# Optimization experiments

Hardware: AMD Instinct MI355X
Metric: run time of the kernel (lower is better)

## Reference

```python
import jax, jax.numpy as jnp
import numpy as np

NBIT = 8


def _qmm(x, W, key):
    """Bit-serial quantized matmul with per-bit noisy weights (faithful to torch quantization()).
    x: (..., in), W: (out, in). Returns z (..., out), min, max, last noisy weight."""
    nsplit = 2 ** NBIT - 1
    mn = jnp.min(x)
    mx = jnp.max(x)
    q = ((x - mn) / (mx - mn) * nsplit).astype(jnp.uint8)  # trunc cast like torch .type(uint8)
    z = jnp.zeros(x.shape[:-1] + (W.shape[0],), x.dtype)
    Wn = W
    for i in range(NBIT):  # fixed 8-bit loop
        noise = jax.random.normal(jax.random.fold_in(key, i), W.shape, W.dtype) * jnp.abs(W) * 0.1
        Wn = W + noise
        bit = ((q >> i) & 1).astype(x.dtype) * float(2 ** i)
        z = z + jnp.matmul(bit, Wn.T)
    return z, mn, mx, Wn  # Wn = weight left in fc after loop (last bit's noisy weight)


def _requant(z, mn, mx, W_last):
    nsplit = 2 ** NBIT - 1
    bias = jnp.sum(mn * W_last, axis=1)  # (out,)
    return z / nsplit * (mx - mn) + bias


def _bn(x2d, gamma, beta, eps=1e-5):
    m = x2d.mean(axis=0)
    v = x2d.var(axis=0)  # biased, like torch BN training normalization
    return (x2d - m) / jnp.sqrt(v + eps) * gamma + beta


def _forward(node_embedding, edge_embedding, nbr_mask, c_two, c_two2, c_three, c_three2,
             bn2_g, bn2_b, bn3_g, bn3_b, nbr_idx):
    B, At, Nbr, Fe = edge_embedding.shape
    Fn = node_embedding.shape[-1]
    gather = jax.vmap(lambda x, i: x[i])  # batched fancy gather along atom axis
    key = jax.random.key(42)

    # two-body
    node_i = jnp.broadcast_to(node_embedding[:, :, None, :], (B, At, Nbr, Fn))
    node_j = gather(node_embedding, nbr_idx) * nbr_mask[..., None]  # (B,At,Nbr,Fn)
    c2 = jnp.concatenate([node_i, node_j], axis=3)  # (B,At,Nbr,2Fn)
    z, mn, mx, Wl = _qmm(c2, c_two, jax.random.fold_in(key, 0))
    c2 = jax.nn.relu(_requant(z, mn, mx, Wl))
    z, mn, mx, Wl = _qmm(c2, c_two2, jax.random.fold_in(key, 1))
    c2 = _requant(z, mn, mx, Wl)
    g2, e2 = jnp.split(c2, 2, axis=3)
    two = jax.nn.sigmoid(g2) * jnp.tanh(e2)
    two = _bn(two.reshape(-1, Fe), bn2_g, bn2_b).reshape(B, At, Nbr, Fe)

    # three-body
    nbr_jk = gather(nbr_idx, nbr_idx)                 # (B,At,Nbr,Nbr) neighbors-of-neighbors
    node_k = gather(node_embedding, nbr_jk)           # (B,At,Nbr,Nbr,Fn)
    edge_jk = gather(edge_embedding, nbr_idx)         # (B,At,Nbr,Nbr,Fe)
    edge_ij = jnp.broadcast_to(edge_embedding[:, :, :, None, :], (B, At, Nbr, Nbr, Fe))
    c3 = jnp.concatenate([
        jnp.broadcast_to(node_i[:, :, :, None, :], (B, At, Nbr, Nbr, Fn)),
        jnp.broadcast_to(node_j[:, :, :, None, :], (B, At, Nbr, Nbr, Fn)),
        node_k, edge_ij, edge_jk], axis=4)            # (B,At,Nbr,Nbr,3Fn+2Fe)
    z, mn, mx, Wl = _qmm(c3, c_three, jax.random.fold_in(key, 2))
    c3 = jax.nn.relu(_requant(z, mn, mx, Wl))
    z, mn, mx, Wl = _qmm(c3, c_three2, jax.random.fold_in(key, 3))
    c3 = _requant(z, mn, mx, Wl)
    g3, e3 = jnp.split(c3, 2, axis=4)
    three = jax.nn.sigmoid(g3) * jnp.tanh(e3)
    mask_jk = gather(nbr_mask, nbr_idx)               # (B,At,Nbr,Nbr) = nbr_mask[b, nbr_idx[b,i,j], k]
    three = (three * mask_jk[..., None]).sum(axis=3)  # (B,At,Nbr,Fe)
    three = _bn(three.reshape(-1, Fe), bn3_g, bn3_b).reshape(B, At, Nbr, Fe)

    return jax.nn.relu(edge_embedding + two + three)


def setup_inputs() -> dict:
    key = jax.random.key(0)
    ks = jax.random.split(key, 8)
    B, At, Nbr, Fn, Fe = 4, 48, 20, 64, 64
    return {
        "node_embedding": jax.random.normal(ks[0], (B, At, Fn), jnp.float32),
        "edge_embedding": jax.random.normal(ks[1], (B, At, Nbr, Fe), jnp.float32),
        "nbr_mask": jnp.ones((B, At, Nbr), jnp.float32),
        "c_two": jax.random.normal(ks[2], (8 * Fn, 2 * Fn), jnp.float32) * 0.05,
        "c_two2": jax.random.normal(ks[3], (2 * Fe, 8 * Fn), jnp.float32) * 0.05,
        "c_three": jax.random.normal(ks[4], (6 * Fn + 4 * Fe, 3 * Fn + 2 * Fe), jnp.float32) * 0.05,
        "c_three2": jax.random.normal(ks[5], (2 * Fe, 6 * Fn + 4 * Fe), jnp.float32) * 0.05,
        "bn2_g": jnp.ones((Fe,), jnp.float32),
        "bn2_b": jnp.zeros((Fe,), jnp.float32),
        "bn3_g": jnp.ones((Fe,), jnp.float32),
        "bn3_b": jnp.zeros((Fe,), jnp.float32),
        "nbr_idx": jax.random.randint(ks[6], (B, At, Nbr), 0, At, jnp.int32),
    }


def reference(node_embedding, edge_embedding, nbr_mask, c_two, c_two2, c_three, c_three2,
              bn2_g, bn2_b, bn3_g, bn3_b, nbr_idx):
    return _forward(node_embedding, edge_embedding, nbr_mask, c_two, c_two2, c_three, c_three2,
                    bn2_g, bn2_b, bn3_g, bn3_b, nbr_idx)
```

## Files before the change

kernel.cpp:

```cpp
#include <hip/hip_runtime.h>
#include <cstdint>
#include <cstddef>

#define DEVI __device__ __forceinline__

typedef __attribute__((ext_vector_type(8))) short s8v;
typedef __attribute__((ext_vector_type(4))) float f4v;

static constexpr int B_ = 4, AT = 48, NBRS = 20;
static constexpr int R2 = B_ * AT * NBRS;
static constexpr int M4 = R2 * NBRS;

static constexpr size_t OFF_B2A  = 0;
static constexpr size_t OFF_B2B  = OFF_B2A + 524288;
static constexpr size_t OFF_B3A  = OFF_B2B + 524288;
static constexpr size_t OFF_BW3B = OFF_B3A + 1638400;
static constexpr size_t OFF_BN3B = OFF_BW3B + 81920;
static constexpr size_t OFF_W72A = OFF_BN3B + 327680;
static constexpr size_t OFF_W72B = OFF_W72A + 65536;
static constexpr size_t OFF_W73A = OFF_W72B + 65536;
static constexpr size_t OFF_W73B = OFF_W73A + 204800;
static constexpr size_t OFF_RS   = OFF_W73B + 81920;
static constexpr size_t OFF_SLOT = OFF_RS + 1408;
static constexpr size_t OFF_BN   = OFF_SLOT + 16;
static constexpr size_t OFF_C2IN = OFF_BN + 256;
static constexpr size_t OFF_Z1   = OFF_C2IN + (size_t)R2 * 128;
static constexpr size_t OFF_C2B  = OFF_Z1 + (size_t)R2 * 512;
static constexpr size_t OFF_Z2   = OFF_C2B + (size_t)R2 * 512;
static constexpr size_t OFF_TWO  = OFF_Z2 + (size_t)R2 * 128;
static constexpr size_t OFF_NK   = OFF_TWO + (size_t)R2 * 64;
static constexpr size_t OFF_P2   = OFF_NK + (size_t)R2 * 64;
static constexpr size_t OFF_P3   = OFF_P2 + (size_t)R2 * 640;
static constexpr size_t OFF_TSUM = OFF_P3 + (size_t)R2 * 640;
static constexpr size_t OFF_Q2A  = OFF_TSUM + (size_t)R2 * 64;
static constexpr size_t OFF_Q2B  = OFF_Q2A + 122880;
static constexpr size_t OFF_QP2  = OFF_Q2B + 491520;
static constexpr size_t OFF_QP3  = OFF_QP2 + 184320;

DEVI void tf2x32(unsigned k0, unsigned k1, unsigned x0, unsigned x1,
                 unsigned& o0, unsigned& o1) {
  unsigned ks0 = k0, ks1 = k1, ks2 = k0 ^ k1 ^ 0x1BD11BDAu;
  x0 += ks0; x1 += ks1;
  const unsigned rotA[4] = {13u, 15u, 26u, 6u};
  const unsigned rotB[4] = {17u, 29u, 16u, 24u};
  unsigned ks[3] = {ks0, ks1, ks2};
  #pragma unroll
  for (int i = 0; i < 5; ++i) {
    const unsigned* rot = (i & 1) ? rotB : rotA;
    #pragma unroll
    for (int r = 0; r < 4; ++r) {
      x0 += x1;
      x1 = (x1 << rot[r]) | (x1 >> (32u - rot[r]));
      x1 ^= x0;
    }
    x0 += ks[(i + 1) % 3];
    x1 += ks[(i + 2) % 3] + (unsigned)(i + 1);
  }
  o0 = x0; o1 = x1;
}

DEVI float erfinv_xla(float x) {
  float w = -log1pf(-x * x);
  float p;
  if (w < 5.f) {
    w -= 2.5f;
    p = 2.81022636e-08f;
    p = fmaf(p, w, 3.43273939e-07f);
    p = fmaf(p, w, -3.5233877e-06f);
    p = fmaf(p, w, -4.39150654e-06f);
    p = fmaf(p, w, 0.00021858087f);
    p = fmaf(p, w, -0.00125372503f);
    p = fmaf(p, w, -0.00417768164f);
    p = fmaf(p, w, 0.246640727f);
    p = fmaf(p, w, 1.50140941f);
  } else {
    w = sqrtf(w) - 3.f;
    p = -0.000200214257f;
    p = fmaf(p, w, 0.000100950558f);
    p = fmaf(p, w, 0.00134934322f);
    p = fmaf(p, w, -0.00367342844f);
    p = fmaf(p, w, 0.00573950773f);
    p = fmaf(p, w, -0.0076224613f);
    p = fmaf(p, w, 0.00943887047f);
    p = fmaf(p, w, 1.00167406f);
    p = fmaf(p, w, 2.83297682f);
  }
  return p * x;
}

DEVI float normal_from_bits(unsigned bits) {
  unsigned fb = (bits >> 9) | 0x3F800000u;
  float f = __uint_as_float(fb) - 1.0f;
  const float lo = -0.99999994f;
  float u = f * (1.0f - lo) + lo;
  u = fmaxf(lo, u);
  return 1.41421356237f * erfinv_xla(u);
}

DEVI unsigned f2o(float f) { unsigned u = __float_as_uint(f); return (u & 0x80000000u) ? ~u : (u | 0x80000000u); }
DEVI float o2f(unsigned u) { return (u & 0x80000000u) ? __uint_as_float(u & 0x7FFFFFFFu) : __uint_as_float(~u); }

DEVI unsigned short f2bf(float x) {
  unsigned u = __float_as_uint(x);
  return (unsigned short)((u + 0x7FFFu + ((u >> 16) & 1u)) >> 16);
}
DEVI float bf2f(unsigned short h) { return __uint_as_float((unsigned)h << 16); }

DEVI void blockMinMax(float lmn, float lmx, float* smem, unsigned* slot) {
  float* smn = smem; float* smx = smem + 256;
  int t = threadIdx.x;
  smn[t] = lmn; smx[t] = lmx;
  __syncthreads();
  for (int s = 128; s > 0; s >>= 1) {
    if (t < s) { smn[t] = fminf(smn[t], smn[t + s]); smx[t] = fmaxf(smx[t], smx[t + s]); }
    __syncthreads();
  }
  if (t == 0) { atomicMin(slot + 0, f2o(smn[0])); atomicMax(slot + 1, f2o(smx[0])); }
}

DEVI s8v expand_mul(unsigned b) {
  unsigned sl = (b & 15u) * 0x00204081u;
  unsigned sh = ((b >> 4) & 15u) * 0x00204081u;
  union { unsigned u[4]; s8v s; } r;
  r.u[0] = (sl & 0x00010001u) * 0x3F80u;
  r.u[1] = ((sl >> 8) & 0x00010001u) * 0x3F80u;
  r.u[2] = (sh & 0x00010001u) * 0x3F80u;
  r.u[3] = ((sh >> 8) & 0x00010001u) * 0x3F80u;
  return r.s;
}
DEVI constexpr int bperm(int bit) { return bit ^ ((((bit) ^ (bit >> 1)) & 1) * 3); }

DEVI s8v bytes_to_bf16(unsigned a, unsigned b) {
  union { unsigned u[4]; s8v s; } r;
  float f0 = (float)(a & 255u), f1 = (float)((a >> 8) & 255u);
  float f2 = (float)((a >> 16) & 255u), f3 = (float)(a >> 24);
  r.u[0] = (__float_as_uint(f0) >> 16) | (__float_as_uint(f1) & 0xFFFF0000u);
  r.u[1] = (__float_as_uint(f2) >> 16) | (__float_as_uint(f3) & 0xFFFF0000u);
  f0 = (float)(b & 255u); f1 = (float)((b >> 8) & 255u);
  f2 = (float)((b >> 16) & 255u); f3 = (float)(b >> 24);
  r.u[2] = (__float_as_uint(f0) >> 16) | (__float_as_uint(f1) & 0xFFFF0000u);
  r.u[3] = (__float_as_uint(f2) >> 16) | (__float_as_uint(f3) & 0xFFFF0000u);
  return r.s;
}

__global__ __launch_bounds__(256) void k_prep(
    const float* __restrict__ W2A, const float* __restrict__ W2B,
    const float* __restrict__ W3A, const float* __restrict__ W3B,
    short* __restrict__ B2A, short* __restrict__ B2B, short* __restrict__ B3A,
    short* __restrict__ BW3B, short* __restrict__ BN3B,
    float* __restrict__ W72A, float* __restrict__ W72B,
    float* __restrict__ W73A, float* __restrict__ W73B,
    float* __restrict__ z1, float* __restrict__ z2, float* __restrict__ tsum,
    unsigned* __restrict__ slots) {
  int t = blockIdx.x * 256 + threadIdx.x;
  if (t < R2 * 512) z1[t] = 0.f;
  if (t < R2 * 128) z2[t] = 0.f;
  if (t < R2 * 64) tsum[t] = 0.f;
  if (t < 4) { slots[2 * t] = f2o(3.402823466e38f); slots[2 * t + 1] = f2o(-3.402823466e38f); }
  int lt = t;
  const float* W; float* W7; int N, K; unsigned layer; int which;
  if (lt < 65536) { W = W2A; W7 = W72A; N = 512; K = 128; layer = 0u; which = 0; }
  else if ((lt -= 65536) < 65536) { W = W2B; W7 = W72B; N = 128; K = 512; layer = 1u; which = 1; }
  else if ((lt -= 65536) < 204800) { W = W3A; W7 = W73A; N = 640; K = 320; layer = 2u; which = 2; }
  else if ((lt -= 204800) < 81920) { W = W3B; W7 = W73B; N = 128; K = 640; layer = 3u; which = 3; }
  else return;
  int e = lt;
  int n = e / K, k = e - n * K;
  float w = W[e];
  float aw = fabsf(w) * 0.1f;
  unsigned kl0, kl1;
  tf2x32(0u, 42u, 0u, layer, kl0, kl1);
  union { short s[8]; s8v v; } hv, lv, bnv;
  #pragma unroll
  for (int bit = 0; bit < 8; ++bit) {
    unsigned kb0, kb1, r0, r1;
    tf2x32(kl0, kl1, 0u, (unsigned)bit, kb0, kb1);
    tf2x32(kb0, kb1, 0u, (unsigned)e, r0, r1);
    float nz = normal_from_bits(r0 ^ r1) * aw;
    float wn = w + nz;
    if (bit == 7) W7[e] = wn;
    if (which == 3) {
      bnv.s[bperm(bit)] = (short)f2bf(ldexpf(nz, bit));
    } else {
      float sv = ldexpf(wn, bit);
      unsigned short hi = f2bf(sv);
      unsigned short lo = f2bf(sv - bf2f(hi));
      hv.s[bperm(bit)] = (short)hi;
      lv.s[bperm(bit)] = (short)lo;
    }
  }
  if (which == 3) {
    *(s8v*)(BN3B + ((size_t)(n >> 4) * 160 + (size_t)(k >> 2)) * 512
                 + (size_t)((k & 3) * 16 + (n & 15)) * 8) = bnv.v;
    unsigned short hi = f2bf(w);
    unsigned short lo = f2bf(w - bf2f(hi));
    size_t o2 = (((size_t)(n >> 4) * 20 + (size_t)(k >> 5)) * 2) * 512
              + (size_t)(((k >> 3) & 3) * 16 + (n & 15)) * 8 + (k & 7);
    BW3B[o2] = (short)hi; BW3B[o2 + 512] = (short)lo;
  } else {
    int pk = k;
    if (which == 2) {
      if (k >= 128 && k < 192) pk = k + 64;
      else if (k >= 192 && k < 256) pk = k - 64;
    }
    short* Bf = (which == 0) ? B2A : (which == 1 ? B2B : B3A);
    int KG = K >> 2;
    size_t off = (((size_t)(n >> 4) * KG + (size_t)(pk >> 2)) * 2) * 512
               + (size_t)((pk & 3) * 16 + (n & 15)) * 8;
    *(s8v*)(Bf + off) = hv.v;
    *(s8v*)(Bf + off + 512) = lv.v;
  }
}

__global__ __launch_bounds__(256) void k_build2(
    const float* __restrict__ node, const float* __restrict__ mask,
    const int* __restrict__ nidx, float* __restrict__ c2in, float* __restrict__ NK,
    const float* __restrict__ W72A, const float* __restrict__ W72B,
    const float* __restrict__ W73A, const float* __restrict__ W73B,
    float* __restrict__ rs, unsigned* __restrict__ slot) {
  __shared__ float sred[512];
  int idx = blockIdx.x * 256 + threadIdx.x;
  float lmn = 3.4e38f, lmx = -3.4e38f;
  if (idx < R2 * 128) {
    int row = idx >> 7, c = idx & 127;
    float v;
    if (c < 64) v = node[(size_t)(row / 20) * 64 + c];
    else {
      int b = row / 960;
      v = node[(size_t)(b * 48 + nidx[row]) * 64 + (c - 64)] * mask[row];
    }
    c2in[idx] = v; lmn = v; lmx = v;
  } else if (idx < R2 * 192) {
    int i2 = idx - R2 * 128;
    int row = i2 >> 6, c = i2 & 63;
    int b = row / 960;
    NK[i2] = node[(size_t)(b * 48 + nidx[row]) * 64 + c];
  } else if (idx < R2 * 192 + 1408) {
    int o = idx - R2 * 192;
    const float* p; int cols; int dsto;
    if (o < 512) { p = W72A; cols = 128; dsto = o; }
    else if (o < 640) { p = W72B; cols = 512; dsto = o; o -= 512; }
    else if (o < 1280) { p = W73A; cols = 320; dsto = o; o -= 640; }
    else { p = W73B; cols = 640; dsto = o; o -= 1280; }
    const float* rowp = p + (size_t)o * cols;
    float s = 0.f;
    for (int j = 0; j < cols; ++j) s += rowp[j];
    rs[dsto] = s;
  }
  blockMinMax(lmn, lmx, sred, slot);
}

__global__ __launch_bounds__(256) void k_qm4(
    const float* __restrict__ node, const float* __restrict__ edge,
    const float* __restrict__ c2in, const float* __restrict__ NK,
    const int* __restrict__ nidx, const unsigned* __restrict__ slot0,
    unsigned char* __restrict__ Q2A, unsigned* __restrict__ slot4) {
  __shared__ float sred[512];
  int idx0 = blockIdx.x * 256 + threadIdx.x;
  if (idx0 < R2 * 128) {
    const float mn = o2f(slot0[0]), mx = o2f(slot0[1]);
    float invd = 255.f / (mx - mn);
    Q2A[idx0] = (unsigned char)((c2in[idx0] - mn) * invd);
  }
  const int n0 = 12288, n1 = n0 + 245760, n2 = n1 + 245760, total = n2 + 4915200;
  float lmn = 3.4e38f, lmx = -3.4e38f;
  for (int idx = idx0; idx < total; idx += gridDim.x * 256) {
    float v, v2;
    if (idx < n0) { v = node[idx]; v2 = v; }
    else if (idx < n1) { v = edge[idx - n0]; v2 = v; }
    else if (idx < n2) {
      int j = idx - n1; int r = j >> 6, c = j & 63;
      v = c2in[(size_t)r * 128 + 64 + c]; v2 = v;
    } else {
      int j = idx - n2; int bij = j / 1280, t = j - bij * 1280;
      int b = bij / 960;
      size_t base = (size_t)((b * 48 + nidx[bij]) * 20) * 64 + t;
      v = NK[base]; v2 = edge[base];
    }
    lmn = fminf(lmn, fminf(v, v2)); lmx = fmaxf(lmx, fmaxf(v, v2));
  }
  blockMinMax(lmn, lmx, sred, slot4);
}

__global__ __launch_bounds__(256) void k_mfma_gemm(
    const unsigned char* __restrict__ Q, int ldq,
    const short* __restrict__ B, int KGfull, int kg0,
    int M, int Nfull, int KB, float* __restrict__ Z, int accflag) {
  const int tid = threadIdx.x;
  const int lane = tid & 63, w = tid >> 6;
  const int l15 = lane & 15, l4 = lane >> 4;
  const int mbase = blockIdx.y * 64;
  const int nbase = blockIdx.x * 128;
  const int kq0 = blockIdx.z * KB;
  f4v acc[4][2];
  #pragma unroll
  for (int a = 0; a < 4; ++a)
    #pragma unroll
    for (int b = 0; b < 2; ++b) acc[a][b] = f4v{0.f, 0.f, 0.f, 0.f};
  for (int ks16 = 0; ks16 < KB; ks16 += 16) {
    uint4 qv[4];
    #pragma unroll
    for (int mf = 0; mf < 4; ++mf)
      qv[mf] = *(const uint4*)(Q + (size_t)(mbase + mf * 16 + l15) * ldq + kq0 + ks16);
    #pragma unroll
    for (int sub = 0; sub < 4; ++sub) {
      int kg = kg0 + ((kq0 + ks16) >> 2) + sub;
      s8v af[4];
      #pragma unroll
      for (int mf = 0; mf < 4; ++mf) {
        unsigned wv = (sub == 0) ? qv[mf].x : (sub == 1) ? qv[mf].y : (sub == 2) ? qv[mf].z : qv[mf].w;
        af[mf] = expand_mul((wv >> (l4 * 8)) & 255u);
      }
      #pragma unroll
      for (int j = 0; j < 2; ++j) {
        size_t o = (((size_t)(nbase / 16 + w * 2 + j) * KGfull + kg) * 2) * 512 + (size_t)lane * 8;
        s8v bh = *(const s8v*)(B + o);
        s8v bl = *(const s8v*)(B + o + 512);
        #pragma unroll
        for (int mf = 0; mf < 4; ++mf) {
          acc[mf][j] = __builtin_amdgcn_mfma_f32_16x16x32_bf16(af[mf], bh, acc[mf][j], 0, 0, 0);
          acc[mf][j] = __builtin_amdgcn_mfma_f32_16x16x32_bf16(af[mf], bl, acc[mf][j], 0, 0, 0);
        }
      }
    }
  }
  #pragma unroll
  for (int mf = 0; mf < 4; ++mf) {
    #pragma unroll
    for (int r = 0; r < 4; ++r) {
      int m = mbase + mf * 16 + l4 * 4 + r;
      float* zp = Z + (size_t)m * Nfull + nbase;
      #pragma unroll
      for (int j = 0; j < 2; ++j) {
        int n = (w * 2 + j) * 16 + l15;
        if (accflag == 0) zp[n] = acc[mf][j][r];
        else atomicAdd(zp + n, acc[mf][j][r]);
      }
    }
  }
}

__global__ __launch_bounds__(256) void k_act1(const float* __restrict__ z1, const float* __restrict__ rs,
                                              const unsigned* __restrict__ slot0,
                                              unsigned* __restrict__ slot1) {
  __shared__ float sred[512];
  const float mn = o2f(slot0[0]), mx = o2f(slot0[1]);
  int idx = blockIdx.x * 256 + threadIdx.x;
  float lmn = 3.4e38f, lmx = -3.4e38f;
  if (idx < R2 * 512) {
    int o = idx & 511;
    float v = fmaxf(0.f, z1[idx] * (1.f / 255.f) * (mx - mn) + mn * rs[o]);
    lmn = v; lmx = v;
  }
  blockMinMax(lmn, lmx, sred, slot1);
}

__global__ __launch_bounds__(256) void k_qq(
    const float* __restrict__ z1, const float* __restrict__ rs,
    const float* __restrict__ node, const float* __restrict__ edge,
    const float* __restrict__ c2in, const float* __restrict__ NK,
    const int* __restrict__ nidx, const unsigned* __restrict__ slot0,
    const unsigned* __restrict__ slot2, const unsigned* __restrict__ slot4,
    unsigned char* __restrict__ Q2B, unsigned char* __restrict__ QP2, unsigned char* __restrict__ QP3) {
  int idx = blockIdx.x * 256 + threadIdx.x;
  if (idx < R2 * 512) {
    const float mn0 = o2f(slot0[0]), mx0 = o2f(slot0[1]);
    const float mn = o2f(slot2[0]), mx = o2f(slot2[1]);
    int o = idx & 511;
    float v = fmaxf(0.f, z1[idx] * (1.f / 255.f) * (mx0 - mn0) + mn0 * rs[o]);
    Q2B[idx] = (unsigned char)((v - mn) * (255.f / (mx - mn)));
    return;
  }
  int j = idx - R2 * 512;
  const int seg = 245760;
  if (j >= 5 * seg) return;
  const float mn = o2f(slot4[0]), mx = o2f(slot4[1]);
  const float invd = 255.f / (mx - mn);
  int s = j / seg; int jj = j - s * seg;
  int r = jj >> 6, c = jj & 63;
  float v; unsigned char* dst;
  if (s == 0)      { v = node[(size_t)(r / 20) * 64 + c];  dst = QP2 + (size_t)r * 192 + c; }
  else if (s == 1) { v = c2in[(size_t)r * 128 + 64 + c];   dst = QP2 + (size_t)r * 192 + 64 + c; }
  else if (s == 2) { v = edge[(size_t)r * 64 + c];         dst = QP2 + (size_t)r * 192 + 128 + c; }
  else if (s == 3) { v = NK[(size_t)r * 64 + c];           dst = QP3 + (size_t)r * 128 + c; }
  else             { v = edge[(size_t)r * 64 + c];         dst = QP3 + (size_t)r * 128 + 64 + c; }
  *dst = (unsigned char)((v - mn) * invd);
}

__global__ __launch_bounds__(256) void k_mfma_p23(
    const unsigned char* __restrict__ Q2, const unsigned char* __restrict__ Q3,
    const short* __restrict__ B, float* __restrict__ P2, float* __restrict__ P3) {
  const int half = blockIdx.y >= 60;
  const int by = blockIdx.y - half * 60;
  const unsigned char* Q = half ? Q3 : Q2;
  float* Z = half ? P3 : P2;
  const int kg0 = half ? 48 : 0;
  const int KB = half ? 128 : 192;
  const int ldq = half ? 128 : 192;
  const int tid = threadIdx.x;
  const int lane = tid & 63, w = tid >> 6;
  const int l15 = lane & 15, l4 = lane >> 4;
  const int mbase = by * 64;
  const int nbase = blockIdx.x * 128;
  f4v acc[4][2];
  #pragma unroll
  for (int a = 0; a < 4; ++a)
    #pragma unroll
    for (int b = 0; b < 2; ++b) acc[a][b] = f4v{0.f, 0.f, 0.f, 0.f};
  for (int ks16 = 0; ks16 < KB; ks16 += 16) {
    uint4 qv[4];
    #pragma unroll
    for (int mf = 0; mf < 4; ++mf)
      qv[mf] = *(const uint4*)(Q + (size_t)(mbase + mf * 16 + l15) * ldq + ks16);
    #pragma unroll
    for (int sub = 0; sub < 4; ++sub) {
      int kg = kg0 + (ks16 >> 2) + sub;
      s8v af[4];
      #pragma unroll
      for (int mf = 0; mf < 4; ++mf) {
        unsigned wv = (sub == 0) ? qv[mf].x : (sub == 1) ? qv[mf].y : (sub == 2) ? qv[mf].z : qv[mf].w;
        af[mf] = expand_mul((wv >> (l4 * 8)) & 255u);
      }
      #pragma unroll
      for (int j = 0; j < 2; ++j) {
        size_t o = (((size_t)(nbase / 16 + w * 2 + j) * 80 + kg) * 2) * 512 + (size_t)lane * 8;
        s8v bh = *(const s8v*)(B + o);
        s8v bl = *(const s8v*)(B + o + 512);
        #pragma unroll
        for (int mf = 0; mf < 4; ++mf) {
          acc[mf][j] = __builtin_amdgcn_mfma_f32_16x16x32_bf16(af[mf], bh, acc[mf][j], 0, 0, 0);
          acc[mf][j] = __builtin_amdgcn_mfma_f32_16x16x32_bf16(af[mf], bl, acc[mf][j], 0, 0, 0);
        }
      }
    }
  }
  #pragma unroll
  for (int mf = 0; mf < 4; ++mf) {
    #pragma unroll
    for (int r = 0; r < 4; ++r) {
      int m = mbase + mf * 16 + l4 * 4 + r;
      float* zp = Z + (size_t)m * 640 + nbase;
      #pragma unroll
      for (int j = 0; j < 2; ++j)
        zp[(w * 2 + j) * 16 + l15] = acc[mf][j][r];
    }
  }
}

__global__ __launch_bounds__(256) void k_act2mm3(
    const float* __restrict__ z2, const float* __restrict__ rs2b,
    const unsigned* __restrict__ slot2, float* __restrict__ two,
    const float* __restrict__ P12, const float* __restrict__ P3,
    const float* __restrict__ rs3a, const int* __restrict__ nidx,
    const unsigned* __restrict__ slot4, unsigned* __restrict__ slot6) {
  __shared__ float p12s[640];
  __shared__ float bias[640];
  __shared__ float sred[512];
  int gid = blockIdx.x * 256 + threadIdx.x;
  if (gid < R2 * 64) {
    const float mn = o2f(slot2[0]), mx = o2f(slot2[1]);
    int row = gid >> 6, c = gid & 63;
    float d = (mx - mn) * (1.f / 255.f);
    float g = z2[(size_t)row * 128 + c] * d + mn * rs2b[c];
    float e = z2[(size_t)row * 128 + 64 + c] * d + mn * rs2b[64 + c];
    two[gid] = (1.f / (1.f + expf(-g))) * tanhf(e);
  }
  const int bij = blockIdx.x;
  const int b = bij / 960;
  const int jp = nidx[bij];
  const size_t p3b = (size_t)((b * 48 + jp) * 20) * 640;
  const float mn2 = o2f(slot4[0]), mx2 = o2f(slot4[1]);
  const float sc2 = (mx2 - mn2) * (1.f / 255.f);
  for (int k = threadIdx.x; k < 640; k += 256) {
    p12s[k] = P12[(size_t)bij * 640 + k];
    bias[k] = mn2 * rs3a[k];
  }
  __syncthreads();
  float lmn = 3.4e38f, lmx = -3.4e38f;
  for (int t = threadIdx.x; t < 20 * 640; t += 256) {
    int knb = t / 640, k = t - knb * 640;
    float v = fmaxf(0.f, (p12s[k] + P3[p3b + t]) * sc2 + bias[k]);
    lmn = fminf(lmn, v); lmx = fmaxf(lmx, v);
  }
  blockMinMax(lmn, lmx, sred, slot6);
}

__global__ __launch_bounds__(256) void k_mfma_l3b(
    const float* __restrict__ P12, const float* __restrict__ P3,
    const float* __restrict__ rs3a, const float* __restrict__ rs3b,
    const short* __restrict__ BW, const short* __restrict__ BN,
    const int* __restrict__ nidx, const float* __restrict__ mask,
    const unsigned* __restrict__ slotA, const unsigned* __restrict__ slotB,
    float* __restrict__ tsum) {
  __shared__ unsigned char qt[64 * 648];
  const int tid = threadIdx.x;
  const int s0 = blockIdx.x * 64;
  const float mn2 = o2f(slotA[0]), mx2 = o2f(slotA[1]);
  const float mn3 = o2f(slotB[0]), mx3 = o2f(slotB[1]);
  const float sc2 = (mx2 - mn2) * (1.f / 255.f);
  const float invd3 = 255.f / (mx3 - mn3);
  {
    int r = tid >> 2, kq = (tid & 3) * 160;
    int s = s0 + r;
    int bij = s / 20, knb = s - bij * 20, b = bij / 960;
    int p3row = (b * 48 + nidx[bij]) * 20 + knb;
    const float* pa = P12 + (size_t)bij * 640;
    const float* pb = P3 + (size_t)p3row * 640;
    for (int k = kq; k < kq + 160; k += 4) {
      float4 va = *(const float4*)(pa + k);
      float4 vb = *(const float4*)(pb + k);
      float4 rv = *(const float4*)(rs3a + k);
      float v0 = fmaxf(0.f, (va.x + vb.x) * sc2 + mn2 * rv.x);
      float v1 = fmaxf(0.f, (va.y + vb.y) * sc2 + mn2 * rv.y);
      float v2 = fmaxf(0.f, (va.z + vb.z) * sc2 + mn2 * rv.z);
      float v3 = fmaxf(0.f, (va.w + vb.w) * sc2 + mn2 * rv.w);
      unsigned pk = (unsigned)((v0 - mn3) * invd3) | ((unsigned)((v1 - mn3) * invd3) << 8)
                  | ((unsigned)((v2 - mn3) * invd3) << 16) | ((unsigned)((v3 - mn3) * invd3) << 24);
      *(unsigned*)(&qt[(size_t)r * 648 + k]) = pk;
    }
  }
  __syncthreads();
  const int lane = tid & 63, wave = tid >> 6;
  const int wm = wave >> 1, wn = wave & 1;
  const int l15 = lane & 15, l4 = lane >> 4;
  const int nfl[4] = {2 * wn, 2 * wn + 1, 2 * wn + 4, 2 * wn + 5};
  size_t bb[4];
  #pragma unroll
  for (int j = 0; j < 4; ++j) bb[j] = ((size_t)nfl[j] * 160) * 512 + (size_t)lane * 8;
  f4v acc[2][4];
  #pragma unroll
  for (int a = 0; a < 2; ++a)
    #pragma unroll
    for (int b = 0; b < 4; ++b) acc[a][b] = f4v{0.f, 0.f, 0.f, 0.f};
  s8v c0[4], c1[4];
  #pragma unroll
  for (int j = 0; j < 4; ++j) {
    c0[j] = *(const s8v*)(BN + bb[j]);
    c1[j] = *(const s8v*)(BN + bb[j] + 512);
  }
  const unsigned char* qrow0 = &qt[(size_t)(wm * 32 + l15) * 648];
  const unsigned char* qrow1 = qrow0 + 16 * 648;
  for (int c = 0; c < 20; ++c) {
    s8v bwh[4];
    #pragma unroll
    for (int j = 0; j < 4; ++j)
      bwh[j] = *(const s8v*)(BW + (((size_t)nfl[j] * 20 + c) * 2) * 512 + (size_t)lane * 8);
    #pragma unroll
    for (int s = 0; s < 8; ++s) {
      const int kg = c * 8 + s;
      unsigned w0 = *(const unsigned*)(qrow0 + kg * 4);
      unsigned w1 = *(const unsigned*)(qrow1 + kg * 4);
      s8v af0 = expand_mul((w0 >> (l4 * 8)) & 255u);
      s8v af1 = expand_mul((w1 >> (l4 * 8)) & 255u);
      s8v nx[4];
      #pragma unroll
      for (int j = 0; j < 4; ++j)
        nx[j] = *(const s8v*)(BN + bb[j] + (size_t)(kg + 2) * 512);
      __builtin_amdgcn_s_setprio(1);
      #pragma unroll
      for (int j = 0; j < 4; ++j) {
        acc[0][j] = __builtin_amdgcn_mfma_f32_16x16x32_bf16(af0, c0[j], acc[0][j], 0, 0, 0);
        acc[1][j] = __builtin_amdgcn_mfma_f32_16x16x32_bf16(af1, c0[j], acc[1][j], 0, 0, 0);
      }
      __builtin_amdgcn_s_setprio(0);
      #pragma unroll
      for (int j = 0; j < 4; ++j) { c0[j] = c1[j]; c1[j] = nx[j]; }
    }
    {
      const int x = c * 32 + l4 * 8;
      unsigned a0 = *(const unsigned*)(qrow0 + x);
      unsigned a1 = *(const unsigned*)(qrow0 + x + 4);
      s8v aq0 = bytes_to_bf16(a0, a1);
      a0 = *(const unsigned*)(qrow1 + x);
      a1 = *(const unsigned*)(qrow1 + x + 4);
      s8v aq1 = bytes_to_bf16(a0, a1);
      __builtin_amdgcn_s_setprio(1);
      #pragma unroll
      for (int j = 0; j < 4; ++j) {
        acc[0][j] = __builtin_amdgcn_mfma_f32_16x16x32_bf16(aq0, bwh[j], acc[0][j], 0, 0, 0);
        acc[1][j] = __builtin_amdgcn_mfma_f32_16x16x32_bf16(aq1, bwh[j], acc[1][j], 0, 0, 0);
        s8v bwl = *(const s8v*)(BW + ((((size_t)nfl[j] * 20 + c) * 2) + 1) * 512 + (size_t)lane * 8);
        acc[0][j] = __builtin_amdgcn_mfma_f32_16x16x32_bf16(aq0, bwl, acc[0][j], 0, 0, 0);
        acc[1][j] = __builtin_amdgcn_mfma_f32_16x16x32_bf16(aq1, bwl, acc[1][j], 0, 0, 0);
      }
      __builtin_amdgcn_s_setprio(0);
    }
  }
  const float d3 = (mx3 - mn3) * (1.f / 255.f);
  float rg[2], re[2];
  #pragma unroll
  for (int j = 0; j < 2; ++j) {
    int gcol = (2 * wn + j) * 16 + l15;
    rg[j] = mn3 * rs3b[gcol];
    re[j] = mn3 * rs3b[64 + gcol];
  }
  #pragma unroll
  for (int mf = 0; mf < 2; ++mf) {
    #pragma unroll
    for (int r = 0; r < 4; ++r) {
      int s = s0 + wm * 32 + mf * 16 + l4 * 4 + r;
      int bij = s / 20, knb = s - bij * 20, b = bij / 960;
      int p3row = (b * 48 + nidx[bij]) * 20 + knb;
      float mk = mask[p3row];
      #pragma unroll
      for (int j = 0; j < 2; ++j) {
        float g = acc[mf][j][r] * d3 + rg[j];
        float e = acc[mf][j + 2][r] * d3 + re[j];
        float val = (1.f / (1.f + expf(-g))) * tanhf(e) * mk;
        atomicAdd(&tsum[(size_t)bij * 64 + (2 * wn + j) * 16 + l15], val);
      }
    }
  }
}

__global__ __launch_bounds__(256) void k_bnstats2(const float* __restrict__ two, const float* __restrict__ tsum,
                                                  float* __restrict__ bn) {
  __shared__ float ss[512];
  const float* x = blockIdx.y ? tsum : two;
  float* mout = bn + (blockIdx.y ? 128 : 0);
  float* vout = mout + 64;
  int c = blockIdx.x, t = threadIdx.x;
  float s = 0.f, q = 0.f;
  for (int r = t; r < R2; r += 256) { float v = x[(size_t)r * 64 + c]; s += v; q += v * v; }
  ss[t] = s; ss[256 + t] = q;
  __syncthreads();
  for (int st = 128; st > 0; st >>= 1) {
    if (t < st) { ss[t] += ss[t + st]; ss[256 + t] += ss[256 + t + st]; }
    __syncthreads();
  }
  if (t == 0) { float m = ss[0] / (float)R2; mout[c] = m; vout[c] = ss[256] / (float)R2 - m * m; }
}

__global__ __launch_bounds__(256) void k_final(const float* __restrict__ edge, const float* __restrict__ two,
                                               const float* __restrict__ tsum, const float* __restrict__ bn,
                                               const float* __restrict__ g2, const float* __restrict__ b2,
                                               const float* __restrict__ g3, const float* __restrict__ b3,
                                               float* __restrict__ out) {
  int idx = blockIdx.x * 256 + threadIdx.x;
  if (idx >= R2 * 64) return;
  int c = idx & 63;
  float t2 = (two[idx] - bn[c]) / sqrtf(bn[64 + c] + 1e-5f) * g2[c] + b2[c];
  float t3 = (tsum[idx] - bn[128 + c]) / sqrtf(bn[192 + c] + 1e-5f) * g3[c] + b3[c];
  out[idx] = fmaxf(0.f, edge[idx] + t2 + t3);
}

extern "C" void kernel_launch(void* const* d_in, const int* in_sizes, int n_in,
                              void* d_out, int out_size, void* d_ws, size_t ws_size,
                              hipStream_t stream) {
  (void)in_sizes; (void)n_in; (void)out_size; (void)ws_size;
  const float* node   = (const float*)d_in[0];
  const float* edge   = (const float*)d_in[1];
  const float* mask   = (const float*)d_in[2];
  const float* c_two  = (const float*)d_in[3];
  const float* c_two2 = (const float*)d_in[4];
  const float* c_three  = (const float*)d_in[5];
  const float* c_three2 = (const float*)d_in[6];
  const float* bn2g = (const float*)d_in[7];
  const float* bn2b = (const float*)d_in[8];
  const float* bn3g = (const float*)d_in[9];
  const float* bn3b = (const float*)d_in[10];
  const int*   nidx = (const int*)d_in[11];
  float* ws = (float*)d_ws;
  unsigned* slots = (unsigned*)(ws + OFF_SLOT);
  float* out = (float*)d_out;
  short* B2A  = (short*)(ws + OFF_B2A);
  short* B2B  = (short*)(ws + OFF_B2B);
  short* B3A  = (short*)(ws + OFF_B3A);
  short* BW3B = (short*)(ws + OFF_BW3B);
  short* BN3B = (short*)(ws + OFF_BN3B);
  unsigned char* Q2A = (unsigned char*)(ws + OFF_Q2A);
  unsigned char* Q2B = (unsigned char*)(ws + OFF_Q2B);
  unsigned char* QP2 = (unsigned char*)(ws + OFF_QP2);
  unsigned char* QP3 = (unsigned char*)(ws + OFF_QP3);
  float* RS = ws + OFF_RS;

  k_prep<<<7680, 256, 0, stream>>>(c_two, c_two2, c_three, c_three2,
                                   B2A, B2B, B3A, BW3B, BN3B,
                                   ws + OFF_W72A, ws + OFF_W72B, ws + OFF_W73A, ws + OFF_W73B,
                                   ws + OFF_Z1, ws + OFF_Z2, ws + OFF_TSUM, slots);
  k_build2<<<2886, 256, 0, stream>>>(node, mask, nidx, ws + OFF_C2IN, ws + OFF_NK,
                                     ws + OFF_W72A, ws + OFF_W72B, ws + OFF_W73A, ws + OFF_W73B,
                                     RS, slots + 0);
  k_qm4<<<2048, 256, 0, stream>>>(node, edge, ws + OFF_C2IN, ws + OFF_NK, nidx, slots + 0,
                                  Q2A, slots + 4);
  k_mfma_gemm<<<dim3(4, 60, 2), 256, 0, stream>>>(Q2A, 128, B2A, 32, 0, 3840, 512, 64, ws + OFF_Z1, 3);
  k_act1<<<7680, 256, 0, stream>>>(ws + OFF_Z1, RS, slots + 0, slots + 2);
  k_qq<<<12480, 256, 0, stream>>>(ws + OFF_Z1, RS, node, edge, ws + OFF_C2IN, ws + OFF_NK,
                                  nidx, slots + 0, slots + 2, slots + 4, Q2B, QP2, QP3);
  k_mfma_gemm<<<dim3(1, 60, 4), 256, 0, stream>>>(Q2B, 512, B2B, 128, 0, 3840, 128, 128, ws + OFF_Z2, 3);
  k_mfma_p23<<<dim3(5, 120), 256, 0, stream>>>(QP2, QP3, B3A, ws + OFF_P2, ws + OFF_P3);
  k_act2mm3<<<3840, 256, 0, stream>>>(ws + OFF_Z2, RS + 512, slots + 2, ws + OFF_TWO,
                                      ws + OFF_P2, ws + OFF_P3, RS + 640, nidx, slots + 4, slots + 6);
  k_mfma_l3b<<<1200, 256, 0, stream>>>(ws + OFF_P2, ws + OFF_P3, RS + 640, RS + 1280,
                                       BW3B, BN3B, nidx, mask, slots + 4, slots + 6, ws + OFF_TSUM);
  k_bnstats2<<<dim3(64, 2), 256, 0, stream>>>(ws + OFF_TWO, ws + OFF_TSUM, ws + OFF_BN);
  k_final<<<960, 256, 0, stream>>>(edge, ws + OFF_TWO, ws + OFF_TSUM, ws + OFF_BN,
                                   bn2g, bn2b, bn3g, bn3b, out);
}
```

Before: 807.6 us.

## Split bit-serial weights into noise-only bf16 and shared hi/lo base for all GEMMs

Applies to the first three quantized matmuls the decomposition already used in layer 3b. Each per-bit noisy weight becomes a noise-only bf16 term per bit plus one shared hi/lo bf16 base weight multiplied by the full byte value. This replaces the old hi+lo MFMA pair for every bit with one MFMA per bit plus a few base MFMAs, roughly halving matrix work. It also merges the p23 kernel into two launches of a generic kernel and removes s_setprio hints in l3b. The cost is one more launch, a different precision profile (the noise term is rounded to bf16 alone), and a changed wave tiling.

```diff
diff --git a/kernel.cpp b/kernel.cpp
--- a/kernel.cpp
+++ b/kernel.cpp
@@ -11,12 +11,15 @@
 static constexpr int R2 = B_ * AT * NBRS;
 static constexpr int M4 = R2 * NBRS;
 
-static constexpr size_t OFF_B2A  = 0;
-static constexpr size_t OFF_B2B  = OFF_B2A + 524288;
-static constexpr size_t OFF_B3A  = OFF_B2B + 524288;
-static constexpr size_t OFF_BW3B = OFF_B3A + 1638400;
-static constexpr size_t OFF_BN3B = OFF_BW3B + 81920;
-static constexpr size_t OFF_W72A = OFF_BN3B + 327680;
+static constexpr size_t OFF_BN2A = 0;
+static constexpr size_t OFF_BW2A = OFF_BN2A + 262144;
+static constexpr size_t OFF_BN2B = OFF_BW2A + 65536;
+static constexpr size_t OFF_BW2B = OFF_BN2B + 262144;
+static constexpr size_t OFF_BN3A = OFF_BW2B + 65536;
+static constexpr size_t OFF_BW3A = OFF_BN3A + 819200;
+static constexpr size_t OFF_BN3B = OFF_BW3A + 204800;
+static constexpr size_t OFF_BW3B = OFF_BN3B + 327680;
+static constexpr size_t OFF_W72A = OFF_BW3B + 81920;
 static constexpr size_t OFF_W72B = OFF_W72A + 65536;
 static constexpr size_t OFF_W73A = OFF_W72B + 65536;
 static constexpr size_t OFF_W73B = OFF_W73A + 204800;
@@ -25,8 +28,7 @@
 static constexpr size_t OFF_BN   = OFF_SLOT + 16;
 static constexpr size_t OFF_C2IN = OFF_BN + 256;
 static constexpr size_t OFF_Z1   = OFF_C2IN + (size_t)R2 * 128;
-static constexpr size_t OFF_C2B  = OFF_Z1 + (size_t)R2 * 512;
-static constexpr size_t OFF_Z2   = OFF_C2B + (size_t)R2 * 512;
+static constexpr size_t OFF_Z2   = OFF_Z1 + (size_t)R2 * 512;
 static constexpr size_t OFF_TWO  = OFF_Z2 + (size_t)R2 * 128;
 static constexpr size_t OFF_NK   = OFF_TWO + (size_t)R2 * 64;
 static constexpr size_t OFF_P2   = OFF_NK + (size_t)R2 * 64;
@@ -146,8 +148,10 @@
 __global__ __launch_bounds__(256) void k_prep(
     const float* __restrict__ W2A, const float* __restrict__ W2B,
     const float* __restrict__ W3A, const float* __restrict__ W3B,
-    short* __restrict__ B2A, short* __restrict__ B2B, short* __restrict__ B3A,
-    short* __restrict__ BW3B, short* __restrict__ BN3B,
+    short* __restrict__ BN2A, short* __restrict__ BW2A,
+    short* __restrict__ BN2B, short* __restrict__ BW2B,
+    short* __restrict__ BN3A, short* __restrict__ BW3A,
+    short* __restrict__ BN3B, short* __restrict__ BW3B,
     float* __restrict__ W72A, float* __restrict__ W72B,
     float* __restrict__ W73A, float* __restrict__ W73B,
     float* __restrict__ z1, float* __restrict__ z2, float* __restrict__ tsum,
@@ -158,11 +162,11 @@
   if (t < R2 * 64) tsum[t] = 0.f;
   if (t < 4) { slots[2 * t] = f2o(3.402823466e38f); slots[2 * t + 1] = f2o(-3.402823466e38f); }
   int lt = t;
-  const float* W; float* W7; int N, K; unsigned layer; int which;
-  if (lt < 65536) { W = W2A; W7 = W72A; N = 512; K = 128; layer = 0u; which = 0; }
-  else if ((lt -= 65536) < 65536) { W = W2B; W7 = W72B; N = 128; K = 512; layer = 1u; which = 1; }
-  else if ((lt -= 65536) < 204800) { W = W3A; W7 = W73A; N = 640; K = 320; layer = 2u; which = 2; }
-  else if ((lt -= 204800) < 81920) { W = W3B; W7 = W73B; N = 128; K = 640; layer = 3u; which = 3; }
+  const float* W; float* W7; short* BNp; short* BWp; int K; unsigned layer; int which;
+  if (lt < 65536) { W = W2A; W7 = W72A; BNp = BN2A; BWp = BW2A; K = 128; layer = 0u; which = 0; }
+  else if ((lt -= 65536) < 65536) { W = W2B; W7 = W72B; BNp = BN2B; BWp = BW2B; K = 512; layer = 1u; which = 1; }
+  else if ((lt -= 65536) < 204800) { W = W3A; W7 = W73A; BNp = BN3A; BWp = BW3A; K = 320; layer = 2u; which = 2; }
+  else if ((lt -= 204800) < 81920) { W = W3B; W7 = W73B; BNp = BN3B; BWp = BW3B; K = 640; layer = 3u; which = 3; }
   else return;
   int e = lt;
   int n = e / K, k = e - n * K;
@@ -170,46 +174,28 @@
   float aw = fabsf(w) * 0.1f;
   unsigned kl0, kl1;
   tf2x32(0u, 42u, 0u, layer, kl0, kl1);
-  union { short s[8]; s8v v; } hv, lv, bnv;
+  union { short s[8]; s8v v; } bnv;
   #pragma unroll
   for (int bit = 0; bit < 8; ++bit) {
     unsigned kb0, kb1, r0, r1;
     tf2x32(kl0, kl1, 0u, (unsigned)bit, kb0, kb1);
     tf2x32(kb0, kb1, 0u, (unsigned)e, r0, r1);
     float nz = normal_from_bits(r0 ^ r1) * aw;
-    float wn = w + nz;
-    if (bit == 7) W7[e] = wn;
-    if (which == 3) {
-      bnv.s[bperm(bit)] = (short)f2bf(ldexpf(nz, bit));
-    } else {
-      float sv = ldexpf(wn, bit);
-      unsigned short hi = f2bf(sv);
-      unsigned short lo = f2bf(sv - bf2f(hi));
-      hv.s[bperm(bit)] = (short)hi;
-      lv.s[bperm(bit)] = (short)lo;
-    }
-  }
-  if (which == 3) {
-    *(s8v*)(BN3B + ((size_t)(n >> 4) * 160 + (size_t)(k >> 2)) * 512
-                 + (size_t)((k & 3) * 16 + (n & 15)) * 8) = bnv.v;
-    unsigned short hi = f2bf(w);
-    unsigned short lo = f2bf(w - bf2f(hi));
-    size_t o2 = (((size_t)(n >> 4) * 20 + (size_t)(k >> 5)) * 2) * 512
-              + (size_t)(((k >> 3) & 3) * 16 + (n & 15)) * 8 + (k & 7);
-    BW3B[o2] = (short)hi; BW3B[o2 + 512] = (short)lo;
-  } else {
-    int pk = k;
-    if (which == 2) {
-      if (k >= 128 && k < 192) pk = k + 64;
-      else if (k >= 192 && k < 256) pk = k - 64;
-    }
-    short* Bf = (which == 0) ? B2A : (which == 1 ? B2B : B3A);
-    int KG = K >> 2;
-    size_t off = (((size_t)(n >> 4) * KG + (size_t)(pk >> 2)) * 2) * 512
-               + (size_t)((pk & 3) * 16 + (n & 15)) * 8;
-    *(s8v*)(Bf + off) = hv.v;
-    *(s8v*)(Bf + off + 512) = lv.v;
-  }
+    if (bit == 7) W7[e] = w + nz;
+    bnv.s[bperm(bit)] = (short)f2bf(ldexpf(nz, bit));
+  }
+  int pk = k;
+  if (which == 2) {
+    if (k >= 128 && k < 192) pk = k + 64;
+    else if (k >= 192 && k < 256) pk = k - 64;
+  }
+  *(s8v*)(BNp + ((size_t)(n >> 4) * (K >> 2) + (size_t)(pk >> 2)) * 512
+              + (size_t)((pk & 3) * 16 + (n & 15)) * 8) = bnv.v;
+  unsigned short hi = f2bf(w);
+  unsigned short lo = f2bf(w - bf2f(hi));
+  size_t o2 = (((size_t)(n >> 4) * (K >> 5) + (size_t)(pk >> 5)) * 2) * 512
+            + (size_t)(((pk >> 3) & 3) * 16 + (n & 15)) * 8 + (pk & 7);
+  BWp[o2] = (short)hi; BWp[o2 + 512] = (short)lo;
 }
 
 __global__ __launch_bounds__(256) void k_build2(
@@ -282,57 +268,93 @@
   blockMinMax(lmn, lmx, sred, slot4);
 }
 
-__global__ __launch_bounds__(256) void k_mfma_gemm(
+__global__ __launch_bounds__(256) void k_nsgemm(
     const unsigned char* __restrict__ Q, int ldq,
-    const short* __restrict__ B, int KGfull, int kg0,
-    int M, int Nfull, int KB, float* __restrict__ Z, int accflag) {
+    const short* __restrict__ BNp, const short* __restrict__ BWp,
+    int KCfull, int c0, int Nfull, int CB,
+    float* __restrict__ Z, int accflag) {
   const int tid = threadIdx.x;
-  const int lane = tid & 63, w = tid >> 6;
+  const int lane = tid & 63, wave = tid >> 6;
+  const int wm = wave >> 1, wn = wave & 1;
   const int l15 = lane & 15, l4 = lane >> 4;
+  const int nfl[4] = {2 * wn, 2 * wn + 1, 2 * wn + 4, 2 * wn + 5};
   const int mbase = blockIdx.y * 64;
   const int nbase = blockIdx.x * 128;
-  const int kq0 = blockIdx.z * KB;
-  f4v acc[4][2];
-  #pragma unroll
-  for (int a = 0; a < 4; ++a)
-    #pragma unroll
-    for (int b = 0; b < 2; ++b) acc[a][b] = f4v{0.f, 0.f, 0.f, 0.f};
-  for (int ks16 = 0; ks16 < KB; ks16 += 16) {
-    uint4 qv[4];
-    #pragma unroll
-    for (int mf = 0; mf < 4; ++mf)
-      qv[mf] = *(const uint4*)(Q + (size_t)(mbase + mf * 16 + l15) * ldq + kq0 + ks16);
-    #pragma unroll
-    for (int sub = 0; sub < 4; ++sub) {
-      int kg = kg0 + ((kq0 + ks16) >> 2) + sub;
-      s8v af[4];
-      #pragma unroll
-      for (int mf = 0; mf < 4; ++mf) {
-        unsigned wv = (sub == 0) ? qv[mf].x : (sub == 1) ? qv[mf].y : (sub == 2) ? qv[mf].z : qv[mf].w;
-        af[mf] = expand_mul((wv >> (l4 * 8)) & 255u);
+  const int cstart = blockIdx.z * CB;
+  size_t bbn[4], bbw[4];
+  #pragma unroll
+  for (int j = 0; j < 4; ++j) {
+    size_t nf = (size_t)(nbase / 16 + nfl[j]);
+    bbn[j] = nf * ((size_t)KCfull * 8) * 512 + (size_t)lane * 8;
+    bbw[j] = nf * (size_t)KCfull * 2 * 512 + (size_t)lane * 8;
+  }
+  const unsigned char* qrow0 = Q + (size_t)(mbase + wm * 32 + l15) * ldq;
+  const unsigned char* qrow1 = qrow0 + (size_t)16 * ldq;
+  f4v acc[2][4];
+  #pragma unroll
+  for (int a = 0; a < 2; ++a)
+    #pragma unroll
+    for (int b = 0; b < 4; ++b) acc[a][b] = f4v{0.f, 0.f, 0.f, 0.f};
+  const int kgs = (cstart + c0) * 8;
+  s8v c0v[4], c1v[4];
+  #pragma unroll
+  for (int j = 0; j < 4; ++j) {
+    c0v[j] = *(const s8v*)(BNp + bbn[j] + (size_t)kgs * 512);
+    c1v[j] = *(const s8v*)(BNp + bbn[j] + (size_t)(kgs + 1) * 512);
+  }
+  for (int cl = 0; cl < CB; ++cl) {
+    const int c = cstart + cl;
+    const int cb = c + c0;
+    s8v bwh[4];
+    #pragma unroll
+    for (int j = 0; j < 4; ++j)
+      bwh[j] = *(const s8v*)(BWp + bbw[j] + (size_t)cb * 2 * 512);
+    #pragma unroll
+    for (int s = 0; s < 8; ++s) {
+      const int kg = cb * 8 + s;
+      unsigned w0 = *(const unsigned*)(qrow0 + c * 32 + s * 4);
+      unsigned w1 = *(const unsigned*)(qrow1 + c * 32 + s * 4);
+      s8v af0 = expand_mul((w0 >> (l4 * 8)) & 255u);
+      s8v af1 = expand_mul((w1 >> (l4 * 8)) & 255u);
+      s8v nx[4];
+      #pragma unroll
+      for (int j = 0; j < 4; ++j)
+        nx[j] = *(const s8v*)(BNp + bbn[j] + (size_t)(kg + 2) * 512);
+      #pragma unroll
+      for (int j = 0; j < 4; ++j) {
+        acc[0][j] = __builtin_amdgcn_mfma_f32_16x16x32_bf16(af0, c0v[j], acc[0][j], 0, 0, 0);
+        acc[1][j] = __builtin_amdgcn_mfma_f32_16x16x32_bf16(af1, c0v[j], acc[1][j], 0, 0, 0);
       }
       #pragma unroll
-      for (int j = 0; j < 2; ++j) {
-        size_t o = (((size_t)(nbase / 16 + w * 2 + j) * KGfull + kg) * 2) * 512 + (size_t)lane * 8;
-        s8v bh = *(const s8v*)(B + o);
-        s8v bl = *(const s8v*)(B + o + 512);
-        #pragma unroll
-        for (int mf = 0; mf < 4; ++mf) {
-          acc[mf][j] = __builtin_amdgcn_mfma_f32_16x16x32_bf16(af[mf], bh, acc[mf][j], 0, 0, 0);
-          acc[mf][j] = __builtin_amdgcn_mfma_f32_16x16x32_bf16(af[mf], bl, acc[mf][j], 0, 0, 0);
-        }
+      for (int j = 0; j < 4; ++j) { c0v[j] = c1v[j]; c1v[j] = nx[j]; }
+    }
+    {
+      const int x = c * 32 + l4 * 8;
+      unsigned a0 = *(const unsigned*)(qrow0 + x);
+      unsigned a1 = *(const unsigned*)(qrow0 + x + 4);
+      s8v aq0 = bytes_to_bf16(a0, a1);
+      a0 = *(const unsigned*)(qrow1 + x);
+      a1 = *(const unsigned*)(qrow1 + x + 4);
+      s8v aq1 = bytes_to_bf16(a0, a1);
+      #pragma unroll
+      for (int j = 0; j < 4; ++j) {
+        acc[0][j] = __builtin_amdgcn_mfma_f32_16x16x32_bf16(aq0, bwh[j], acc[0][j], 0, 0, 0);
+        acc[1][j] = __builtin_amdgcn_mfma_f32_16x16x32_bf16(aq1, bwh[j], acc[1][j], 0, 0, 0);
+        s8v bwl = *(const s8v*)(BWp + bbw[j] + ((size_t)cb * 2 + 1) * 512);
+        acc[0][j] = __builtin_amdgcn_mfma_f32_16x16x32_bf16(aq0, bwl, acc[0][j], 0, 0, 0);
+        acc[1][j] = __builtin_amdgcn_mfma_f32_16x16x32_bf16(aq1, bwl, acc[1][j], 0, 0, 0);
       }
     }
   }
   #pragma unroll
-  for (int mf = 0; mf < 4; ++mf) {
+  for (int mf = 0; mf < 2; ++mf) {
     #pragma unroll
     for (int r = 0; r < 4; ++r) {
-      int m = mbase + mf * 16 + l4 * 4 + r;
+      int m = mbase + wm * 32 + mf * 16 + l4 * 4 + r;
       float* zp = Z + (size_t)m * Nfull + nbase;
       #pragma unroll
-      for (int j = 0; j < 2; ++j) {
-        int n = (w * 2 + j) * 16 + l15;
+      for (int j = 0; j < 4; ++j) {
+        int n = nfl[j] * 16 + l15;
         if (accflag == 0) zp[n] = acc[mf][j][r];
         else atomicAdd(zp + n, acc[mf][j][r]);
       }
@@ -385,66 +407,6 @@
   else if (s == 3) { v = NK[(size_t)r * 64 + c];           dst = QP3 + (size_t)r * 128 + c; }
   else             { v = edge[(size_t)r * 64 + c];         dst = QP3 + (size_t)r * 128 + 64 + c; }
   *dst = (unsigned char)((v - mn) * invd);
-}
-
-__global__ __launch_bounds__(256) void k_mfma_p23(
-    const unsigned char* __restrict__ Q2, const unsigned char* __restrict__ Q3,
-    const short* __restrict__ B, float* __restrict__ P2, float* __restrict__ P3) {
-  const int half = blockIdx.y >= 60;
-  const int by = blockIdx.y - half * 60;
-  const unsigned char* Q = half ? Q3 : Q2;
-  float* Z = half ? P3 : P2;
-  const int kg0 = half ? 48 : 0;
-  const int KB = half ? 128 : 192;
-  const int ldq = half ? 128 : 192;
-  const int tid = threadIdx.x;
-  const int lane = tid & 63, w = tid >> 6;
-  const int l15 = lane & 15, l4 = lane >> 4;
-  const int mbase = by * 64;
-  const int nbase = blockIdx.x * 128;
-  f4v acc[4][2];
-  #pragma unroll
-  for (int a = 0; a < 4; ++a)
-    #pragma unroll
-    for (int b = 0; b < 2; ++b) acc[a][b] = f4v{0.f, 0.f, 0.f, 0.f};
-  for (int ks16 = 0; ks16 < KB; ks16 += 16) {
-    uint4 qv[4];
-    #pragma unroll
-    for (int mf = 0; mf < 4; ++mf)
-      qv[mf] = *(const uint4*)(Q + (size_t)(mbase + mf * 16 + l15) * ldq + ks16);
-    #pragma unroll
-    for (int sub = 0; sub < 4; ++sub) {
-      int kg = kg0 + (ks16 >> 2) + sub;
-      s8v af[4];
-      #pragma unroll
-      for (int mf = 0; mf < 4; ++mf) {
-        unsigned wv = (sub == 0) ? qv[mf].x : (sub == 1) ? qv[mf].y : (sub == 2) ? qv[mf].z : qv[mf].w;
-        af[mf] = expand_mul((wv >> (l4 * 8)) & 255u);
-      }
-      #pragma unroll
-      for (int j = 0; j < 2; ++j) {
-        size_t o = (((size_t)(nbase / 16 + w * 2 + j) * 80 + kg) * 2) * 512 + (size_t)lane * 8;
-        s8v bh = *(const s8v*)(B + o);
-        s8v bl = *(const s8v*)(B + o + 512);
-        #pragma unroll
-        for (int mf = 0; mf < 4; ++mf) {
-          acc[mf][j] = __builtin_amdgcn_mfma_f32_16x16x32_bf16(af[mf], bh, acc[mf][j], 0, 0, 0);
-          acc[mf][j] = __builtin_amdgcn_mfma_f32_16x16x32_bf16(af[mf], bl, acc[mf][j], 0, 0, 0);
-        }
-      }
-    }
-  }
-  #pragma unroll
-  for (int mf = 0; mf < 4; ++mf) {
-    #pragma unroll
-    for (int r = 0; r < 4; ++r) {
-      int m = mbase + mf * 16 + l4 * 4 + r;
-      float* zp = Z + (size_t)m * 640 + nbase;
-      #pragma unroll
-      for (int j = 0; j < 2; ++j)
-        zp[(w * 2 + j) * 16 + l15] = acc[mf][j][r];
-    }
-  }
 }
 
 __global__ __launch_bounds__(256) void k_act2mm3(
@@ -556,13 +518,11 @@
       #pragma unroll
       for (int j = 0; j < 4; ++j)
         nx[j] = *(const s8v*)(BN + bb[j] + (size_t)(kg + 2) * 512);
-      __builtin_amdgcn_s_setprio(1);
       #pragma unroll
       for (int j = 0; j < 4; ++j) {
         acc[0][j] = __builtin_amdgcn_mfma_f32_16x16x32_bf16(af0, c0[j], acc[0][j], 0, 0, 0);
         acc[1][j] = __builtin_amdgcn_mfma_f32_16x16x32_bf16(af1, c0[j], acc[1][j], 0, 0, 0);
       }
-      __builtin_amdgcn_s_setprio(0);
       #pragma unroll
       for (int j = 0; j < 4; ++j) { c0[j] = c1[j]; c1[j] = nx[j]; }
     }
@@ -574,7 +534,6 @@
       a0 = *(const unsigned*)(qrow1 + x);
       a1 = *(const unsigned*)(qrow1 + x + 4);
       s8v aq1 = bytes_to_bf16(a0, a1);
-      __builtin_amdgcn_s_setprio(1);
       #pragma unroll
       for (int j = 0; j < 4; ++j) {
         acc[0][j] = __builtin_amdgcn_mfma_f32_16x16x32_bf16(aq0, bwh[j], acc[0][j], 0, 0, 0);
@@ -583,7 +542,6 @@
         acc[0][j] = __builtin_amdgcn_mfma_f32_16x16x32_bf16(aq0, bwl, acc[0][j], 0, 0, 0);
         acc[1][j] = __builtin_amdgcn_mfma_f32_16x16x32_bf16(aq1, bwl, acc[1][j], 0, 0, 0);
       }
-      __builtin_amdgcn_s_setprio(0);
     }
   }
   const float d3 = (mx3 - mn3) * (1.f / 255.f);
@@ -663,11 +621,10 @@
   float* ws = (float*)d_ws;
   unsigned* slots = (unsigned*)(ws + OFF_SLOT);
   float* out = (float*)d_out;
-  short* B2A  = (short*)(ws + OFF_B2A);
-  short* B2B  = (short*)(ws + OFF_B2B);
-  short* B3A  = (short*)(ws + OFF_B3A);
-  short* BW3B = (short*)(ws + OFF_BW3B);
-  short* BN3B = (short*)(ws + OFF_BN3B);
+  short* BN2A = (short*)(ws + OFF_BN2A); short* BW2A = (short*)(ws + OFF_BW2A);
+  short* BN2B = (short*)(ws + OFF_BN2B); short* BW2B = (short*)(ws + OFF_BW2B);
+  short* BN3A = (short*)(ws + OFF_BN3A); short* BW3A = (short*)(ws + OFF_BW3A);
+  short* BN3B = (short*)(ws + OFF_BN3B); short* BW3B = (short*)(ws + OFF_BW3B);
   unsigned char* Q2A = (unsigned char*)(ws + OFF_Q2A);
   unsigned char* Q2B = (unsigned char*)(ws + OFF_Q2B);
   unsigned char* QP2 = (unsigned char*)(ws + OFF_QP2);
@@ -675,7 +632,7 @@
   float* RS = ws + OFF_RS;
 
   k_prep<<<7680, 256, 0, stream>>>(c_two, c_two2, c_three, c_three2,
-                                   B2A, B2B, B3A, BW3B, BN3B,
+                                   BN2A, BW2A, BN2B, BW2B, BN3A, BW3A, BN3B, BW3B,
                                    ws + OFF_W72A, ws + OFF_W72B, ws + OFF_W73A, ws + OFF_W73B,
                                    ws + OFF_Z1, ws + OFF_Z2, ws + OFF_TSUM, slots);
   k_build2<<<2886, 256, 0, stream>>>(node, mask, nidx, ws + OFF_C2IN, ws + OFF_NK,
@@ -683,12 +640,13 @@
                                      RS, slots + 0);
   k_qm4<<<2048, 256, 0, stream>>>(node, edge, ws + OFF_C2IN, ws + OFF_NK, nidx, slots + 0,
                                   Q2A, slots + 4);
-  k_mfma_gemm<<<dim3(4, 60, 2), 256, 0, stream>>>(Q2A, 128, B2A, 32, 0, 3840, 512, 64, ws + OFF_Z1, 3);
+  k_nsgemm<<<dim3(4, 60, 2), 256, 0, stream>>>(Q2A, 128, BN2A, BW2A, 4, 0, 512, 2, ws + OFF_Z1, 3);
   k_act1<<<7680, 256, 0, stream>>>(ws + OFF_Z1, RS, slots + 0, slots + 2);
   k_qq<<<12480, 256, 0, stream>>>(ws + OFF_Z1, RS, node, edge, ws + OFF_C2IN, ws + OFF_NK,
                                   nidx, slots + 0, slots + 2, slots + 4, Q2B, QP2, QP3);
-  k_mfma_gemm<<<dim3(1, 60, 4), 256, 0, stream>>>(Q2B, 512, B2B, 128, 0, 3840, 128, 128, ws + OFF_Z2, 3);
-  k_mfma_p23<<<dim3(5, 120), 256, 0, stream>>>(QP2, QP3, B3A, ws + OFF_P2, ws + OFF_P3);
+  k_nsgemm<<<dim3(1, 60, 4), 256, 0, stream>>>(Q2B, 512, BN2B, BW2B, 16, 0, 128, 4, ws + OFF_Z2, 3);
+  k_nsgemm<<<dim3(5, 60, 1), 256, 0, stream>>>(QP2, 192, BN3A, BW3A, 10, 0, 640, 6, ws + OFF_P2, 0);
+  k_nsgemm<<<dim3(5, 60, 1), 256, 0, stream>>>(QP3, 128, BN3A, BW3A, 10, 6, 640, 4, ws + OFF_P3, 0);
   k_act2mm3<<<3840, 256, 0, stream>>>(ws + OFF_Z2, RS + 512, slots + 2, ws + OFF_TWO,
                                       ws + OFF_P2, ws + OFF_P3, RS + 640, nidx, slots + 4, slots + 6);
   k_mfma_l3b<<<1200, 256, 0, stream>>>(ws + OFF_P2, ws + OFF_P3, RS + 640, RS + 1280,
```

Measured after the change: 798.8 us. No clear change (-1.1%).
